# Optimization experiments

Measured on AMD Instinct MI355X. Metric: run time of the kernel, lower is better.

Reference implementation:

```python
import jax, jax.numpy as jnp
import numpy as np

NUM_CLUSTERS = 64
NUM_ITERS = 3
TEMPERATURE = 0.1
CENTER_EMA = 0.99


def _l2norm(x, eps=1e-12):
    n = jnp.linalg.norm(x, axis=-1, keepdims=True)
    return x / jnp.maximum(n, eps)


def setup_inputs() -> dict:
    key = jax.random.key(0)
    k1, k2 = jax.random.split(key)
    B, N, d = 16, 4096, 768
    features = jax.random.normal(k1, (B, N, d), dtype=jnp.float32)
    centers = jax.random.normal(k2, (NUM_CLUSTERS, d), dtype=jnp.float32)
    return {"features": features, "centers": centers}


def reference(features, centers):
    B, N, d = features.shape
    K = centers.shape[0]
    M = B * N  # single-device: M_total == M_local

    features_norm = _l2norm(features)          # [B, N, d]
    centers_n = _l2norm(centers)               # [K, d]

    logits = jnp.einsum('bnd,kd->bnk', features_norm, centers_n) / TEMPERATURE
    Q = jnp.exp(logits.astype(jnp.float32).reshape(M, K).T)  # [K, M]

    Q = Q / jnp.maximum(Q.sum(), 1e-12)
    for _ in range(NUM_ITERS):
        row_sums = Q.sum(axis=1, keepdims=True)              # [K, 1]
        Q = Q / (jnp.maximum(row_sums, 1e-12) * float(K))
        col_sums = Q.sum(axis=0, keepdims=True)              # [1, M]
        Q = Q / (jnp.maximum(col_sums, 1e-12) * float(M))

    assignments = (Q * float(M)).T.reshape(B, N, K).astype(features.dtype)

    # EMA center update
    Q_flat = assignments.reshape(M, K)
    feat_flat = features_norm.reshape(M, d)
    weighted = jnp.einsum('mk,md->kd', Q_flat, feat_flat)    # [K, d]
    mass = Q_flat.sum(axis=0)                                # [K]
    new_centers = _l2norm(weighted / jnp.maximum(mass, 1e-6)[:, None])
    updated = CENTER_EMA * centers_n + (1.0 - CENTER_EMA) * new_centers
    updated = _l2norm(updated)

    return assignments, updated
```

## Files before the change

### kernel.cpp

```cpp
#include <hip/hip_runtime.h>
#include <hip/hip_bf16.h>

#define M_TOTAL 65536
#define DIM 768
#define KC 64
#define INV_T 10.0f

#define DT 128
#define MB 64
#define CH 8
#define MSEG 128

#define LOGITS_BLOCKS (M_TOTAL / 64)
#define SROWS 128
#define SINK_BLOCKS (M_TOTAL / SROWS)

typedef __attribute__((ext_vector_type(4))) float f32x4;
typedef __attribute__((ext_vector_type(8))) short bf16x8;
typedef __attribute__((ext_vector_type(4))) unsigned short u16x4;

__device__ __forceinline__ short f2bf(float f) {
    __hip_bfloat16 h = __float2bfloat16(f);
    union { __hip_bfloat16 h; short s; } u; u.h = h;
    return u.s;
}

__global__ __launch_bounds__(256) void k_centers(const float* __restrict__ centers,
                                                 float* __restrict__ cn,
                                                 short* __restrict__ cnbf) {
    int k = blockIdx.x, tid = threadIdx.x;
    float ss = 0.f;
    for (int i = tid; i < DIM; i += 256) { float v = centers[k * DIM + i]; ss += v * v; }
    __shared__ float red[4];
    for (int o = 32; o; o >>= 1) ss += __shfl_xor(ss, o);
    if ((tid & 63) == 0) red[tid >> 6] = ss;
    __syncthreads();
    ss = red[0] + red[1] + red[2] + red[3];
    float inv = 1.0f / fmaxf(sqrtf(ss), 1e-12f);
    for (int i = tid; i < DIM; i += 256) {
        float v = centers[k * DIM + i] * inv;
        cn[k * DIM + i] = v;
        cnbf[k * DIM + i] = f2bf(v);
    }
}

__global__ __launch_bounds__(256) void k_logits(const float* __restrict__ F,
                                                const short* __restrict__ cnbf,
                                                float* __restrict__ E,
                                                float* __restrict__ invn,
                                                float* __restrict__ PS0) {
    __shared__ float fbuf[2][4096];
    __shared__ float bsr[4][KC];
    int tid = threadIdx.x;
    int wave = tid >> 6, lane = tid & 63;
    int l15 = lane & 15, lhi = lane >> 4;
    int rowbase = blockIdx.x * 64;

    int srow = tid >> 4;
    int c4 = (tid & 15) * 4;

    f32x4 acc[4];
#pragma unroll
    for (int n = 0; n < 4; ++n) acc[n] = (f32x4){0.f, 0.f, 0.f, 0.f};
    float ss = 0.f;

    auto stage = [&](int t, int b) {
#pragma unroll
        for (int i = 0; i < 4; ++i) {
            int row = i * 16 + srow;
            const float* src = F + (size_t)(rowbase + row) * DIM + t * 64 + (c4 ^ ((row & 7) << 2));
            float* dst = &fbuf[b][i * 1024 + wave * 256];
            __builtin_amdgcn_global_load_lds((const __attribute__((address_space(1))) void*)src,
                                             (__attribute__((address_space(3))) void*)dst, 16, 0, 0);
        }
    };

    stage(0, 0);
    __syncthreads();

    int myrow = wave * 16 + l15;
    int swz = (l15 & 7) << 2;
    const short* Bb = cnbf + (size_t)l15 * DIM + lhi * 8;

    for (int t = 0; t < 12; ++t) {
        int cur = t & 1;
        if (t < 11) stage(t + 1, cur ^ 1);
        const float* cb = fbuf[cur] + myrow * 64;
#pragma unroll
        for (int kk = 0; kk < 64; kk += 32) {
            int c0s = (kk + lhi * 8) ^ swz;
            f32x4 fa = *(const f32x4*)(cb + c0s);
            f32x4 fb2 = *(const f32x4*)(cb + (c0s ^ 4));
            ss += fa[0] * fa[0] + fa[1] * fa[1] + fa[2] * fa[2] + fa[3] * fa[3]
                + fb2[0] * fb2[0] + fb2[1] * fb2[1] + fb2[2] * fb2[2] + fb2[3] * fb2[3];
            bf16x8 af;
            af[0] = f2bf(fa[0]); af[1] = f2bf(fa[1]); af[2] = f2bf(fa[2]); af[3] = f2bf(fa[3]);
            af[4] = f2bf(fb2[0]); af[5] = f2bf(fb2[1]); af[6] = f2bf(fb2[2]); af[7] = f2bf(fb2[3]);
#pragma unroll
            for (int n = 0; n < 4; ++n) {
                bf16x8 b = *(const bf16x8*)(Bb + (size_t)n * 16 * DIM + t * 64 + kk);
                acc[n] = __builtin_amdgcn_mfma_f32_16x16x32_bf16(af, b, acc[n], 0, 0, 0);
            }
        }
        __syncthreads();
    }

    ss += __shfl_xor(ss, 16);
    ss += __shfl_xor(ss, 32);
    float inv = 1.0f / fmaxf(sqrtf(ss), 1e-12f);
    int growbase = rowbase + wave * 16;
    if (lane < 16) invn[growbase + lane] = inv;

    float sc[4];
#pragma unroll
    for (int j = 0; j < 4; ++j) sc[j] = __shfl(inv, lhi * 4 + j) * INV_T;

    float colp[4] = {0.f, 0.f, 0.f, 0.f};
#pragma unroll
    for (int n = 0; n < 4; ++n) {
#pragma unroll
        for (int j = 0; j < 4; ++j) {
            float e = expf(acc[n][j] * sc[j]);
            int row = lhi * 4 + j;
            E[(size_t)(growbase + row) * KC + ((n * 16 + l15) ^ (row << 2))] = e;
            colp[n] += e;
        }
    }
#pragma unroll
    for (int n = 0; n < 4; ++n) {
        colp[n] += __shfl_xor(colp[n], 16);
        colp[n] += __shfl_xor(colp[n], 32);
    }
    if (lane < 16) {
#pragma unroll
        for (int n = 0; n < 4; ++n) bsr[wave][n * 16 + lane] = colp[n];
    }
    __syncthreads();
    if (tid < KC) PS0[(size_t)blockIdx.x * KC + tid] =
        bsr[0][tid] + bsr[1][tid] + bsr[2][tid] + bsr[3][tid];
}

template <int MODE>
__global__ __launch_bounds__(256) void k_sink(const float* __restrict__ E,
                                              const float* __restrict__ Rprev,
                                              const float* __restrict__ PSprev,
                                              const float* __restrict__ invn,
                                              float* __restrict__ c,
                                              float* __restrict__ PS,
                                              float* __restrict__ Rout,
                                              float* __restrict__ Aout,
                                              short* __restrict__ Qbf) {
    __shared__ float tile[SROWS * KC];
    __shared__ float sbuf[SROWS];
    __shared__ float Rlds[KC];
    __shared__ float bacc[4][KC];
    int tid = threadIdx.x, lane = tid & 63, wave = tid >> 6;
    int m0 = blockIdx.x * SROWS;

#pragma unroll
    for (int i = 0; i < 8; ++i) {
        const float* src = E + (size_t)(m0 + i * 16 + wave * 4 + (lane >> 4)) * KC + (lane & 15) * 4;
        float* dst = tile + (i * 16 + wave * 4) * KC;
        __builtin_amdgcn_global_load_lds((const __attribute__((address_space(1))) void*)src,
                                         (__attribute__((address_space(3))) void*)dst, 16, 0, 0);
    }

    {
        constexpr int NB = (MODE == 0) ? LOGITS_BLOCKS : SINK_BLOCKS;
        int k = tid & 63, g = tid >> 6;
        float s = 0.f;
#pragma unroll 8
        for (int p = g; p < NB; p += 4) s += PSprev[(size_t)p * KC + k];
        bacc[g][k] = s;
        __syncthreads();
        if (tid < KC) {
            float sk = bacc[0][k] + bacc[1][k] + bacc[2][k] + bacc[3][k];
            float r;
            if (MODE == 0) {
                float tot = sk;
                for (int o = 32; o; o >>= 1) tot += __shfl_xor(tot, o);
                float S = fmaxf(tot, 1e-12f);
                r = (1.0f / S) / (fmaxf(sk / S, 1e-12f) * 64.0f);
            } else {
                float rp = Rprev[k];
                r = rp / (fmaxf(rp * sk, 1e-12f) * 64.0f);
            }
            Rlds[k] = r;
            if (MODE != 2) Rout[k] = r;
        }
    }
    __syncthreads();

    if (tid < SROWS) {
        const float* rp = tile + tid * KC;
        const f32x4* R4 = (const f32x4*)Rlds;
        int sw = tid & 15;
        f32x4 a = {0.f, 0.f, 0.f, 0.f};
#pragma unroll
        for (int j = 0; j < 16; ++j)
            a += *(const f32x4*)(rp + ((j ^ sw) << 2)) * R4[j];
        sbuf[tid] = a[0] + a[1] + a[2] + a[3];
    }
    __syncthreads();

    float Rl = Rlds[lane];
    float wacc = 0.f;
    int rbase = wave * 32;
#pragma unroll 4
    for (int r = 0; r < 32; ++r) {
        int rr = rbase + r;
        int m = m0 + rr;
        float e = tile[rr * KC + (lane ^ ((rr & 15) << 2))];
        float s = sbuf[rr];
        float cold = (MODE == 0) ? 1.0f : c[m];
        float cnew = cold / (fmaxf(cold * s, 1e-12f) * 65536.0f);
        if (MODE == 2) {
            float a = e * Rl * cnew * 65536.0f;
            size_t idx = (size_t)m * KC + lane;
            Aout[idx] = a;
            Qbf[idx] = f2bf(a * invn[m]);
            wacc += a;
        } else {
            if (lane == 0) c[m] = cnew;
            wacc += e * cnew;
        }
    }
    bacc[wave][lane] = wacc;
    __syncthreads();
    if (tid < KC) PS[(size_t)blockIdx.x * KC + tid] =
        bacc[0][tid] + bacc[1][tid] + bacc[2][tid] + bacc[3][tid];
}

__global__ __launch_bounds__(256) void k_weighted(const float* __restrict__ F,
                                                  const short* __restrict__ Qbf,
                                                  float* __restrict__ P) {
    __shared__ short ldsF[DT * MB];
    __shared__ short ldsQ[KC * MB];
    int tid = threadIdx.x;
    int dt = blockIdx.x;
    int ms = blockIdx.y;
    int wave = tid >> 6, lane = tid & 63;
    int l15 = lane & 15, lhi = lane >> 4;

    int m0 = ms * (MB * CH);
    int d0 = dt * DT;

    f32x4 acc[4][2];
#pragma unroll
    for (int kt = 0; kt < 4; ++kt)
#pragma unroll
        for (int ds = 0; ds < 2; ++ds) acc[kt][ds] = (f32x4){0.f, 0.f, 0.f, 0.f};

    int f_dq = (tid & 31) * 4;
    int f_m8 = (tid >> 5) * 8;
    int q_kq = (tid & 15) * 4;
    int q_m8 = ((tid >> 4) & 7) * 8;

    float4 rf[8];
    u16x4 q[8];
#define LOADCH(mb_)                                                                       \
    do {                                                                                  \
        _Pragma("unroll") for (int j = 0; j < 8; ++j)                                     \
            rf[j] = *(const float4*)(F + (size_t)((mb_) + f_m8 + j) * DIM + d0 + f_dq);   \
        if (tid < 128) {                                                                  \
            _Pragma("unroll") for (int j = 0; j < 8; ++j)                                 \
                q[j] = *(const u16x4*)(Qbf + (size_t)((mb_) + q_m8 + j) * KC + q_kq);     \
        }                                                                                 \
    } while (0)

    LOADCH(m0);
    for (int ch = 0; ch < CH; ++ch) {
        __syncthreads();
#pragma unroll
        for (int i = 0; i < 4; ++i) {
            int d = f_dq + i;
            uint4 w;
            w.x = (unsigned)(unsigned short)f2bf(rf[0][i]) | ((unsigned)(unsigned short)f2bf(rf[1][i]) << 16);
            w.y = (unsigned)(unsigned short)f2bf(rf[2][i]) | ((unsigned)(unsigned short)f2bf(rf[3][i]) << 16);
            w.z = (unsigned)(unsigned short)f2bf(rf[4][i]) | ((unsigned)(unsigned short)f2bf(rf[5][i]) << 16);
            w.w = (unsigned)(unsigned short)f2bf(rf[6][i]) | ((unsigned)(unsigned short)f2bf(rf[7][i]) << 16);
            int byte = (d * (MB * 2) + f_m8 * 2) ^ ((d & 7) << 4);
            *(uint4*)((char*)ldsF + byte) = w;
        }
        if (tid < 128) {
#pragma unroll
            for (int i = 0; i < 4; ++i) {
                int k = q_kq + i;
                uint4 w;
                w.x = (unsigned)q[0][i] | ((unsigned)q[1][i] << 16);
                w.y = (unsigned)q[2][i] | ((unsigned)q[3][i] << 16);
                w.z = (unsigned)q[4][i] | ((unsigned)q[5][i] << 16);
                w.w = (unsigned)q[6][i] | ((unsigned)q[7][i] << 16);
                int byte = (k * (MB * 2) + q_m8 * 2) ^ ((k & 7) << 4);
                *(uint4*)((char*)ldsQ + byte) = w;
            }
        }
        __syncthreads();
        if (ch + 1 < CH) LOADCH(m0 + (ch + 1) * MB);
#pragma unroll
        for (int h = 0; h < 2; ++h) {
            bf16x8 afr[4];
#pragma unroll
            for (int kt = 0; kt < 4; ++kt) {
                int k = kt * 16 + l15;
                int byte = (k * (MB * 2) + (h * 32 + lhi * 8) * 2) ^ ((k & 7) << 4);
                afr[kt] = *(bf16x8*)((char*)ldsQ + byte);
            }
#pragma unroll
            for (int ds = 0; ds < 2; ++ds) {
                int d = wave * 32 + ds * 16 + l15;
                int byte = (d * (MB * 2) + (h * 32 + lhi * 8) * 2) ^ ((d & 7) << 4);
                bf16x8 bfr = *(bf16x8*)((char*)ldsF + byte);
#pragma unroll
                for (int kt = 0; kt < 4; ++kt)
                    acc[kt][ds] = __builtin_amdgcn_mfma_f32_16x16x32_bf16(afr[kt], bfr, acc[kt][ds], 0, 0, 0);
            }
        }
    }
#undef LOADCH

    float* Pb = P + (size_t)ms * (KC * DIM) + d0;
#pragma unroll
    for (int kt = 0; kt < 4; ++kt)
#pragma unroll
        for (int ds = 0; ds < 2; ++ds) {
            int d = wave * 32 + ds * 16 + l15;
#pragma unroll
            for (int r4 = 0; r4 < 4; ++r4) {
                int k = kt * 16 + lhi * 4 + r4;
                Pb[(size_t)k * DIM + d] = acc[kt][ds][r4];
            }
        }
}

__global__ __launch_bounds__(256) void k_final(const float* __restrict__ P,
                                               const float* __restrict__ PSM,
                                               const float* __restrict__ cn,
                                               float* __restrict__ outC) {
    int k = blockIdx.x, tid = threadIdx.x;
    __shared__ float red[4];

    float msum = 0.f;
    for (int p = tid; p < SINK_BLOCKS; p += 256) msum += PSM[(size_t)p * KC + k];
    for (int o = 32; o; o >>= 1) msum += __shfl_xor(msum, o);
    if ((tid & 63) == 0) red[tid >> 6] = msum;
    __syncthreads();
    float mk = fmaxf(red[0] + red[1] + red[2] + red[3], 1e-6f);
    __syncthreads();

    float w[3];
#pragma unroll
    for (int g = 0; g < 3; ++g) {
        int d = tid + g * 256;
        const float* pp = P + (size_t)k * DIM + d;
        float s0 = 0.f, s1 = 0.f, s2 = 0.f, s3 = 0.f;
        size_t stride = (size_t)KC * DIM;
#pragma unroll 4
        for (int msg = 0; msg < MSEG; msg += 4) {
            s0 += pp[(size_t)msg * stride];
            s1 += pp[(size_t)(msg + 1) * stride];
            s2 += pp[(size_t)(msg + 2) * stride];
            s3 += pp[(size_t)(msg + 3) * stride];
        }
        w[g] = ((s0 + s1) + (s2 + s3)) / mk;
    }

    float ss = w[0] * w[0] + w[1] * w[1] + w[2] * w[2];
    for (int o = 32; o; o >>= 1) ss += __shfl_xor(ss, o);
    if ((tid & 63) == 0) red[tid >> 6] = ss;
    __syncthreads();
    ss = red[0] + red[1] + red[2] + red[3];
    float n1 = fmaxf(sqrtf(ss), 1e-12f);
    __syncthreads();

    float u0 = 0.99f * cn[k * DIM + tid]       + 0.01f * (w[0] / n1);
    float u1 = 0.99f * cn[k * DIM + tid + 256] + 0.01f * (w[1] / n1);
    float u2 = 0.99f * cn[k * DIM + tid + 512] + 0.01f * (w[2] / n1);
    float ss2 = u0 * u0 + u1 * u1 + u2 * u2;
    for (int o = 32; o; o >>= 1) ss2 += __shfl_xor(ss2, o);
    if ((tid & 63) == 0) red[tid >> 6] = ss2;
    __syncthreads();
    ss2 = red[0] + red[1] + red[2] + red[3];
    float n2 = fmaxf(sqrtf(ss2), 1e-12f);

    outC[k * DIM + tid]       = u0 / n2;
    outC[k * DIM + tid + 256] = u1 / n2;
    outC[k * DIM + tid + 512] = u2 / n2;
}

extern "C" void kernel_launch(void* const* d_in, const int* in_sizes, int n_in,
                              void* d_out, int out_size, void* d_ws, size_t ws_size,
                              hipStream_t stream) {
    const float* F = (const float*)d_in[0];
    const float* centers = (const float*)d_in[1];
    float* out = (float*)d_out;
    float* A = out;
    float* outC = out + (size_t)M_TOTAL * KC;

    float* w = (float*)d_ws;
    float* cn   = w;
    short* cnbf = (short*)(w + 49152);
    float* R0   = w + 73728;
    float* R1   = w + 73792;
    float* invn = w + 74048;
    float* cbuf = w + 139584;
    float* E    = w + 205120;
    short* Qbf  = (short*)(w + 4399424);
    float* PS0  = w + 6496576;
    float* PS1  = w + 6562112;
    float* PS2  = w + 6594880;
    float* PSM  = w + 6627648;
    float* partial = w + 6660416;

    k_centers<<<KC, 256, 0, stream>>>(centers, cn, cnbf);
    k_logits<<<LOGITS_BLOCKS, 256, 0, stream>>>(F, cnbf, E, invn, PS0);
    k_sink<0><<<SINK_BLOCKS, 256, 0, stream>>>(E, nullptr, PS0, invn, cbuf, PS1, R0, A, Qbf);
    k_sink<1><<<SINK_BLOCKS, 256, 0, stream>>>(E, R0, PS1, invn, cbuf, PS2, R1, A, Qbf);
    k_sink<2><<<SINK_BLOCKS, 256, 0, stream>>>(E, R1, PS2, invn, cbuf, PSM, nullptr, A, Qbf);

    dim3 wgrid(DIM / DT, MSEG);
    k_weighted<<<wgrid, 256, 0, stream>>>(F, Qbf, partial);
    k_final<<<KC, 256, 0, stream>>>(partial, PSM, cn, outC);
}
```

Measured before the change: 192.9 us.

## Make logits staging per-wave with triple buffering and vmcnt waits instead of barriers

The logits kernel now has each wave stage only its own 16 feature rows into LDS, using a three-deep buffer and prefetching two tiles ahead. Block-wide __syncthreads is replaced by explicit s_waitcnt vmcnt waits. Center bf16 fragments are loaded before the MFMA loop, and the t loop is fully unrolled. The intent is to hide global-load latency and drop barrier stalls, at the cost of more LDS (three buffers) and more registers. Correctness now depends on the vmcnt counts matching exactly the outstanding loads.

```diff
diff --git a/kernel.cpp b/kernel.cpp
--- a/kernel.cpp
+++ b/kernel.cpp
@@ -49,46 +49,59 @@
                                                 float* __restrict__ E,
                                                 float* __restrict__ invn,
                                                 float* __restrict__ PS0) {
-    __shared__ float fbuf[2][4096];
+    __shared__ float fbuf[3][4][1024];
     __shared__ float bsr[4][KC];
     int tid = threadIdx.x;
     int wave = tid >> 6, lane = tid & 63;
     int l15 = lane & 15, lhi = lane >> 4;
     int rowbase = blockIdx.x * 64;
 
-    int srow = tid >> 4;
-    int c4 = (tid & 15) * 4;
+    int srow_l = lane >> 4;
+    int c4 = lane & 15;
+
+#define STAGE(t_, b_)                                                                     \
+    do {                                                                                  \
+        _Pragma("unroll") for (int i_ = 0; i_ < 4; ++i_) {                                \
+            int r_ = i_ * 4 + srow_l;                                \
+            const float* src_ = F + (size_t)(rowbase + wave * 16 + r_) * DIM + (t_) * 64  \
+                                + (((c4 ^ (r_ & 7)) << 2));                               \
+            float* dst_ = &fbuf[b_][wave][i_ * 256];                                      \
+            __builtin_amdgcn_global_load_lds(                                             \
+                (const __attribute__((address_space(1))) void*)src_,                      \
+                (__attribute__((address_space(3))) void*)dst_, 16, 0, 0);                 \
+        }                                                                                 \
+    } while (0)
+
+    STAGE(0, 0);
+    STAGE(1, 1);
 
     f32x4 acc[4];
 #pragma unroll
     for (int n = 0; n < 4; ++n) acc[n] = (f32x4){0.f, 0.f, 0.f, 0.f};
     float ss = 0.f;
 
-    auto stage = [&](int t, int b) {
-#pragma unroll
-        for (int i = 0; i < 4; ++i) {
-            int row = i * 16 + srow;
-            const float* src = F + (size_t)(rowbase + row) * DIM + t * 64 + (c4 ^ ((row & 7) << 2));
-            float* dst = &fbuf[b][i * 1024 + wave * 256];
-            __builtin_amdgcn_global_load_lds((const __attribute__((address_space(1))) void*)src,
-                                             (__attribute__((address_space(3))) void*)dst, 16, 0, 0);
-        }
-    };
-
-    stage(0, 0);
-    __syncthreads();
-
-    int myrow = wave * 16 + l15;
+    const short* Bb = cnbf + (size_t)l15 * DIM + lhi * 8;
     int swz = (l15 & 7) << 2;
-    const short* Bb = cnbf + (size_t)l15 * DIM + lhi * 8;
-
+
+#pragma unroll
     for (int t = 0; t < 12; ++t) {
-        int cur = t & 1;
-        if (t < 11) stage(t + 1, cur ^ 1);
-        const float* cb = fbuf[cur] + myrow * 64;
-#pragma unroll
-        for (int kk = 0; kk < 64; kk += 32) {
-            int c0s = (kk + lhi * 8) ^ swz;
+        bf16x8 b[8];
+#pragma unroll
+        for (int n = 0; n < 4; ++n) {
+            b[n * 2]     = *(const bf16x8*)(Bb + (size_t)n * 16 * DIM + t * 64);
+            b[n * 2 + 1] = *(const bf16x8*)(Bb + (size_t)n * 16 * DIM + t * 64 + 32);
+        }
+        if (t + 2 < 12) {
+            STAGE(t + 2, (t + 2) % 3);
+            asm volatile("s_waitcnt vmcnt(4)" ::: "memory");
+        } else {
+            asm volatile("s_waitcnt vmcnt(0)" ::: "memory");
+        }
+        __builtin_amdgcn_sched_barrier(0);
+        const float* cb = &fbuf[t % 3][wave][l15 * 64];
+#pragma unroll
+        for (int kk = 0; kk < 2; ++kk) {
+            int c0s = (kk * 32 + lhi * 8) ^ swz;
             f32x4 fa = *(const f32x4*)(cb + c0s);
             f32x4 fb2 = *(const f32x4*)(cb + (c0s ^ 4));
             ss += fa[0] * fa[0] + fa[1] * fa[1] + fa[2] * fa[2] + fa[3] * fa[3]
@@ -97,13 +110,11 @@
             af[0] = f2bf(fa[0]); af[1] = f2bf(fa[1]); af[2] = f2bf(fa[2]); af[3] = f2bf(fa[3]);
             af[4] = f2bf(fb2[0]); af[5] = f2bf(fb2[1]); af[6] = f2bf(fb2[2]); af[7] = f2bf(fb2[3]);
 #pragma unroll
-            for (int n = 0; n < 4; ++n) {
-                bf16x8 b = *(const bf16x8*)(Bb + (size_t)n * 16 * DIM + t * 64 + kk);
-                acc[n] = __builtin_amdgcn_mfma_f32_16x16x32_bf16(af, b, acc[n], 0, 0, 0);
-            }
-        }
-        __syncthreads();
-    }
+            for (int n = 0; n < 4; ++n)
+                acc[n] = __builtin_amdgcn_mfma_f32_16x16x32_bf16(af, b[n * 2 + kk], acc[n], 0, 0, 0);
+        }
+    }
+#undef STAGE
 
     ss += __shfl_xor(ss, 16);
     ss += __shfl_xor(ss, 32);
```

Measured after the change: 181.4 us. 1.06x faster.
